# Optimization experiments

Measured on AMD Instinct MI355X. Metric: run time of the kernel, lower is better.

The kernel has to match this reference:

```python
import jax, jax.numpy as jnp
import numpy as np

B, T, D, H = 32, 8192, 128, 128

def setup_inputs() -> dict:
    key = jax.random.key(0)
    k1, k2, k3, k4, k5 = jax.random.split(key, 5)
    return {
        "encoder_outputs": jax.random.normal(k1, (B, T, D), dtype=jnp.float32),
        "decoder_hidden": jax.random.normal(k2, (B, H), dtype=jnp.float32),
        "W1": jax.random.normal(k3, (D, D), dtype=jnp.float32) * 0.08,
        "W2": jax.random.normal(k4, (H, D), dtype=jnp.float32) * 0.08,
        "V": jax.random.normal(k5, (D, 1), dtype=jnp.float32) * 0.08,
    }

def reference(encoder_outputs, decoder_hidden, W1, W2, V):
    # score: [B, T, D] = tanh(enc @ W1 + (dec @ W2)[:, None, :])
    score = jnp.tanh(jnp.einsum('btd,de->bte', encoder_outputs, W1)
                     + jnp.einsum('bh,hd->bd', decoder_hidden, W2)[:, None, :])
    # logits: [B, T, 1]; softmax over time axis (axis=1)
    logits = jnp.einsum('btd,do->bto', score, V)
    attention_weights = jax.nn.softmax(logits, axis=1)
    # context: [B, D] weighted sum over T
    context_vector = jnp.sum(attention_weights * encoder_outputs, axis=1)
    return context_vector, attention_weights
```

## Files before the change

### kernel.cpp

```cpp
#include <hip/hip_runtime.h>

#define B_ 32
#define T_ 8192
#define D_ 128
#define MBLK 128
#define NCHUNK 64

typedef __attribute__((ext_vector_type(8))) _Float16 half8;
typedef __attribute__((ext_vector_type(4))) _Float16 half4;
typedef __attribute__((ext_vector_type(4))) float floatx4;

__device__ __forceinline__ float tanh_fast(float x) {
    float e = __expf(2.0f * x);
    return 1.0f - __fdividef(2.0f, e + 1.0f);
}

__global__ void prep_kernel(const float* __restrict__ W1, half8* __restrict__ W1frag,
                            const float* __restrict__ dec, const float* __restrict__ W2,
                            float* __restrict__ bias) {
    int bid = blockIdx.x, tid = threadIdx.x;
    if (bid < 8) {
        int tg = bid * 256 + tid;
        int kk = tg >> 9, ni = (tg >> 6) & 7, lane = tg & 63;
        half8 h;
        #pragma unroll
        for (int j = 0; j < 8; ++j) {
            int k = kk * 32 + ((lane >> 4) * 8) + j;
            int n = ni * 16 + (lane & 15);
            h[j] = (_Float16)W1[k * 128 + n];
        }
        W1frag[tg] = h;
    } else {
        int b = (bid - 8) * 2 + (tid >> 7);
        int d = tid & 127;
        float acc = 0.f;
        for (int h = 0; h < 128; ++h)
            acc += dec[b * 128 + h] * W2[h * 128 + d];
        bias[b * 128 + d] = acc;
    }
}

__global__ __launch_bounds__(512, 4)
void main_kernel(const float* __restrict__ enc, const half8* __restrict__ W1frag,
                 const float* __restrict__ bias, const float* __restrict__ V,
                 float* __restrict__ out_w, float* __restrict__ m_part,
                 float* __restrict__ s_part, float* __restrict__ c_part)
{
    __shared__ __align__(16) _Float16 encl[MBLK * 128];
    __shared__ __align__(16) half8 bfr[2048];
    __shared__ float red[MBLK];
    __shared__ float c_red[16][128];

    const int tid = threadIdx.x;
    const int l = tid & 63;
    const int w = tid >> 6;
    const int bid = blockIdx.x;
    const int b = bid >> 6;
    const int chunk = bid & 63;
    const float* encp = enc + ((long)(b * T_) + chunk * MBLK) * D_;

    #pragma unroll
    for (int q = 0; q < 4; ++q)
        bfr[q * 512 + tid] = W1frag[q * 512 + tid];

    const int arow = w * 16 + (l & 15);
    const float* rowp = encp + arow * 128 + ((l >> 4) * 8);
    half8 afr[4];
    #pragma unroll
    for (int kk = 0; kk < 4; ++kk) {
        float4 f0 = *(const float4*)(rowp + kk * 32);
        float4 f1 = *(const float4*)(rowp + kk * 32 + 4);
        half8 a;
        a[0] = (_Float16)f0.x; a[1] = (_Float16)f0.y;
        a[2] = (_Float16)f0.z; a[3] = (_Float16)f0.w;
        a[4] = (_Float16)f1.x; a[5] = (_Float16)f1.y;
        a[6] = (_Float16)f1.z; a[7] = (_Float16)f1.w;
        afr[kk] = a;
    }
    __syncthreads();

    floatx4 acc[8];
    #pragma unroll
    for (int ni = 0; ni < 8; ++ni) acc[ni] = (floatx4)0.0f;

    #pragma unroll
    for (int kk = 0; kk < 4; ++kk)
        #pragma unroll
        for (int ni = 0; ni < 8; ++ni)
            acc[ni] = __builtin_amdgcn_mfma_f32_16x16x32_f16(
                          afr[kk], bfr[(kk * 8 + ni) * 64 + l], acc[ni], 0, 0, 0);

    {
        const int asw = (arow & 7) << 4;
        #pragma unroll
        for (int kk = 0; kk < 4; ++kk) {
            int byte = arow * 256 + (((kk * 64) + ((l >> 4) * 16)) ^ asw);
            *(half8*)((char*)encl + byte) = afr[kk];
        }
    }

    float bs[8], vv[8];
    #pragma unroll
    for (int ni = 0; ni < 8; ++ni) {
        int n = ni * 16 + (l & 15);
        bs[ni] = bias[b * 128 + n];
        vv[ni] = V[n];
    }
    #pragma unroll
    for (int j2 = 0; j2 < 4; ++j2) {
        float p = 0.f;
        #pragma unroll
        for (int ni = 0; ni < 8; ++ni)
            p += tanh_fast(acc[ni][j2] + bs[ni]) * vv[ni];
        #pragma unroll
        for (int mk = 1; mk < 16; mk <<= 1)
            p += __shfl_xor(p, mk);
        if ((l & 15) == 0) {
            int r = w * 16 + (l >> 4) * 4 + j2;
            red[r] = p;
            out_w[(long)b * T_ + chunk * MBLK + r] = p;
        }
    }
    __syncthreads();

    float l0 = red[l], l1 = red[l + 64];
    float m = fmaxf(l0, l1);
    #pragma unroll
    for (int mk = 1; mk < 64; mk <<= 1) m = fmaxf(m, __shfl_xor(m, mk));
    {
        float e0 = __expf(l0 - m), e1 = __expf(l1 - m);
        float s = e0 + e1;
        #pragma unroll
        for (int mk = 1; mk < 64; mk <<= 1) s += __shfl_xor(s, mk);
        if (tid == 0) { m_part[bid] = m; s_part[bid] = s; }
    }

    {
        int dg = tid & 31, rg = tid >> 5;
        floatx4 cc = (floatx4)0.0f;
        #pragma unroll
        for (int rr = 0; rr < 8; ++rr) {
            int r = rg * 8 + rr;
            float wgt = __expf(red[r] - m);
            half4 h = *(const half4*)((char*)encl +
                       (r * 256 + ((dg * 8) ^ ((r & 7) << 4))));
            #pragma unroll
            for (int i = 0; i < 4; ++i) cc[i] += wgt * (float)h[i];
        }
        *(floatx4*)(&c_red[rg][dg * 4]) = cc;
    }
    __syncthreads();
    if (tid < 128) {
        float s = 0.f;
        #pragma unroll
        for (int g = 0; g < 16; ++g) s += c_red[g][tid];
        c_part[(long)bid * 128 + tid] = s;
    }
}

__global__ void reduce_kernel(const float* __restrict__ m_part, const float* __restrict__ s_part,
                              const float* __restrict__ c_part, float* __restrict__ ctx,
                              float* __restrict__ mg, float* __restrict__ sg)
{
    __shared__ float sm[64];
    __shared__ float sc[64];
    int b = blockIdx.x, i = threadIdx.x;
    float m = m_part[b * 64 + i];
    sm[i] = m;
    __syncthreads();
    for (int s = 32; s > 0; s >>= 1) {
        if (i < s) sm[i] = fmaxf(sm[i], sm[i + s]);
        __syncthreads();
    }
    float m_g = sm[0];
    __syncthreads();
    float e = __expf(m - m_g);
    sm[i] = s_part[b * 64 + i] * e;
    __syncthreads();
    for (int s = 32; s > 0; s >>= 1) {
        if (i < s) sm[i] += sm[i + s];
        __syncthreads();
    }
    float s_g = sm[0];
    __syncthreads();
    sc[i] = e / s_g;
    if (i == 0) { mg[b] = m_g; sg[b] = s_g; }
    __syncthreads();
    float acc0 = 0.f, acc1 = 0.f;
    for (int ch = 0; ch < 64; ++ch) {
        float w = sc[ch];
        acc0 += c_part[((long)b * 64 + ch) * 128 + i] * w;
        acc1 += c_part[((long)b * 64 + ch) * 128 + 64 + i] * w;
    }
    ctx[b * 128 + i] = acc0;
    ctx[b * 128 + 64 + i] = acc1;
}

__global__ void finalize_kernel(float* __restrict__ out_w, const float* __restrict__ mg,
                                const float* __restrict__ sg)
{
    int idx = blockIdx.x * 256 + threadIdx.x;
    int b = idx >> 13;
    float lg = out_w[idx];
    out_w[idx] = __expf(lg - mg[b]) / sg[b];
}

extern "C" void kernel_launch(void* const* d_in, const int* in_sizes, int n_in,
                              void* d_out, int out_size, void* d_ws, size_t ws_size,
                              hipStream_t stream)
{
    const float* enc = (const float*)d_in[0];
    const float* dec = (const float*)d_in[1];
    const float* W1  = (const float*)d_in[2];
    const float* W2  = (const float*)d_in[3];
    const float* V   = (const float*)d_in[4];

    float* ctx  = (float*)d_out;
    float* outw = ctx + B_ * D_;

    float* ws     = (float*)d_ws;
    float* bias   = ws;
    float* m_part = bias + 4096;
    float* s_part = m_part + 2048;
    float* mg     = s_part + 2048;
    float* sg     = mg + 32;
    float* c_part = sg + 32;
    half8* W1frag = (half8*)(c_part + (long)B_ * NCHUNK * 128);

    prep_kernel<<<24, 256, 0, stream>>>(W1, W1frag, dec, W2, bias);
    main_kernel<<<B_ * NCHUNK, 512, 0, stream>>>(enc, W1frag, bias, V, outw, m_part, s_part, c_part);
    reduce_kernel<<<B_, 64, 0, stream>>>(m_part, s_part, c_part, ctx, mg, sg);
    finalize_kernel<<<(B_ * T_) / 256, 256, 0, stream>>>(outw, mg, sg);
}
```

Baseline: 54.62 us.

## Drop LDS staging of encoder tile, fuse finalize into reduce kernel

The context accumulation now uses the fp16 A fragments already held in registers, reduced with cross-lane shuffles, so the 32KB LDS copy of the encoder tile and its swizzled write/read are removed. Global loads of enc, W1 fragments and bias are issued before a single barrier. The finalize kernel is folded into the reduce kernel, which uses wave shuffles instead of LDS tree reductions and saves one launch. This cuts LDS use and may raise occupancy, at the cost of more shuffle instructions and only 32 blocks doing the attention-weight normalization pass.

```diff
diff --git a/kernel.cpp b/kernel.cpp
--- a/kernel.cpp
+++ b/kernel.cpp
@@ -7,7 +7,6 @@
 #define NCHUNK 64
 
 typedef __attribute__((ext_vector_type(8))) _Float16 half8;
-typedef __attribute__((ext_vector_type(4))) _Float16 half4;
 typedef __attribute__((ext_vector_type(4))) float floatx4;
 
 __device__ __forceinline__ float tanh_fast(float x) {
@@ -40,31 +39,27 @@
     }
 }
 
-__global__ __launch_bounds__(512, 4)
+__global__ __launch_bounds__(512)
 void main_kernel(const float* __restrict__ enc, const half8* __restrict__ W1frag,
                  const float* __restrict__ bias, const float* __restrict__ V,
                  float* __restrict__ out_w, float* __restrict__ m_part,
                  float* __restrict__ s_part, float* __restrict__ c_part)
 {
-    __shared__ __align__(16) _Float16 encl[MBLK * 128];
     __shared__ __align__(16) half8 bfr[2048];
-    __shared__ float red[MBLK];
-    __shared__ float c_red[16][128];
+    __shared__ __align__(16) float red[MBLK];
+    __shared__ __align__(16) float c_red[8][128];
 
     const int tid = threadIdx.x;
     const int l = tid & 63;
     const int w = tid >> 6;
+    const int g = l >> 4;
     const int bid = blockIdx.x;
     const int b = bid >> 6;
     const int chunk = bid & 63;
     const float* encp = enc + ((long)(b * T_) + chunk * MBLK) * D_;
 
-    #pragma unroll
-    for (int q = 0; q < 4; ++q)
-        bfr[q * 512 + tid] = W1frag[q * 512 + tid];
-
     const int arow = w * 16 + (l & 15);
-    const float* rowp = encp + arow * 128 + ((l >> 4) * 8);
+    const float* rowp = encp + arow * 128 + g * 8;
     half8 afr[4];
     #pragma unroll
     for (int kk = 0; kk < 4; ++kk) {
@@ -77,27 +72,10 @@
         a[6] = (_Float16)f1.z; a[7] = (_Float16)f1.w;
         afr[kk] = a;
     }
-    __syncthreads();
-
-    floatx4 acc[8];
-    #pragma unroll
-    for (int ni = 0; ni < 8; ++ni) acc[ni] = (floatx4)0.0f;
-
-    #pragma unroll
-    for (int kk = 0; kk < 4; ++kk)
-        #pragma unroll
-        for (int ni = 0; ni < 8; ++ni)
-            acc[ni] = __builtin_amdgcn_mfma_f32_16x16x32_f16(
-                          afr[kk], bfr[(kk * 8 + ni) * 64 + l], acc[ni], 0, 0, 0);
-
-    {
-        const int asw = (arow & 7) << 4;
-        #pragma unroll
-        for (int kk = 0; kk < 4; ++kk) {
-            int byte = arow * 256 + (((kk * 64) + ((l >> 4) * 16)) ^ asw);
-            *(half8*)((char*)encl + byte) = afr[kk];
-        }
-    }
+
+    #pragma unroll
+    for (int q = 0; q < 4; ++q)
+        bfr[q * 512 + tid] = W1frag[q * 512 + tid];
 
     float bs[8], vv[8];
     #pragma unroll
@@ -106,20 +84,35 @@
         bs[ni] = bias[b * 128 + n];
         vv[ni] = V[n];
     }
+    __syncthreads();
+
+    floatx4 acc[8];
+    #pragma unroll
+    for (int ni = 0; ni < 8; ++ni) acc[ni] = (floatx4)0.0f;
+
+    #pragma unroll
+    for (int kk = 0; kk < 4; ++kk)
+        #pragma unroll
+        for (int ni = 0; ni < 8; ++ni)
+            acc[ni] = __builtin_amdgcn_mfma_f32_16x16x32_f16(
+                          afr[kk], bfr[(kk * 8 + ni) * 64 + l], acc[ni], 0, 0, 0);
+
+    float p[4];
     #pragma unroll
     for (int j2 = 0; j2 < 4; ++j2) {
-        float p = 0.f;
+        float q = 0.f;
         #pragma unroll
         for (int ni = 0; ni < 8; ++ni)
-            p += tanh_fast(acc[ni][j2] + bs[ni]) * vv[ni];
+            q += tanh_fast(acc[ni][j2] + bs[ni]) * vv[ni];
         #pragma unroll
         for (int mk = 1; mk < 16; mk <<= 1)
-            p += __shfl_xor(p, mk);
-        if ((l & 15) == 0) {
-            int r = w * 16 + (l >> 4) * 4 + j2;
-            red[r] = p;
-            out_w[(long)b * T_ + chunk * MBLK + r] = p;
-        }
+            q += __shfl_xor(q, mk);
+        p[j2] = q;
+    }
+    if ((l & 15) == 0) {
+        floatx4 v4 = {p[0], p[1], p[2], p[3]};
+        *(floatx4*)(&red[w * 16 + g * 4]) = v4;
+        *(floatx4*)(out_w + (long)b * T_ + chunk * MBLK + w * 16 + g * 4) = v4;
     }
     __syncthreads();
 
@@ -128,81 +121,76 @@
     #pragma unroll
     for (int mk = 1; mk < 64; mk <<= 1) m = fmaxf(m, __shfl_xor(m, mk));
     {
-        float e0 = __expf(l0 - m), e1 = __expf(l1 - m);
-        float s = e0 + e1;
+        float s = __expf(l0 - m) + __expf(l1 - m);
         #pragma unroll
         for (int mk = 1; mk < 64; mk <<= 1) s += __shfl_xor(s, mk);
         if (tid == 0) { m_part[bid] = m; s_part[bid] = s; }
     }
 
     {
-        int dg = tid & 31, rg = tid >> 5;
-        floatx4 cc = (floatx4)0.0f;
-        #pragma unroll
-        for (int rr = 0; rr < 8; ++rr) {
-            int r = rg * 8 + rr;
-            float wgt = __expf(red[r] - m);
-            half4 h = *(const half4*)((char*)encl +
-                       (r * 256 + ((dg * 8) ^ ((r & 7) << 4))));
+        float wgt = __expf(red[arow] - m);
+        #pragma unroll
+        for (int kk = 0; kk < 4; ++kk) {
+            float cc[8];
             #pragma unroll
-            for (int i = 0; i < 4; ++i) cc[i] += wgt * (float)h[i];
+            for (int j = 0; j < 8; ++j) {
+                cc[j] = wgt * (float)afr[kk][j];
+                #pragma unroll
+                for (int mk = 1; mk < 16; mk <<= 1)
+                    cc[j] += __shfl_xor(cc[j], mk);
+            }
+            if ((l & 15) == 0) {
+                floatx4 v0 = {cc[0], cc[1], cc[2], cc[3]};
+                floatx4 v1 = {cc[4], cc[5], cc[6], cc[7]};
+                *(floatx4*)(&c_red[w][kk * 32 + g * 8]) = v0;
+                *(floatx4*)(&c_red[w][kk * 32 + g * 8 + 4]) = v1;
+            }
         }
-        *(floatx4*)(&c_red[rg][dg * 4]) = cc;
     }
     __syncthreads();
     if (tid < 128) {
         float s = 0.f;
         #pragma unroll
-        for (int g = 0; g < 16; ++g) s += c_red[g][tid];
+        for (int ww = 0; ww < 8; ++ww) s += c_red[ww][tid];
         c_part[(long)bid * 128 + tid] = s;
     }
 }
 
-__global__ void reduce_kernel(const float* __restrict__ m_part, const float* __restrict__ s_part,
-                              const float* __restrict__ c_part, float* __restrict__ ctx,
-                              float* __restrict__ mg, float* __restrict__ sg)
+__global__ __launch_bounds__(256)
+void reduce_kernel(const float* __restrict__ m_part, const float* __restrict__ s_part,
+                   const float* __restrict__ c_part, float* __restrict__ ctx,
+                   float* __restrict__ out_w)
 {
-    __shared__ float sm[64];
     __shared__ float sc[64];
-    int b = blockIdx.x, i = threadIdx.x;
-    float m = m_part[b * 64 + i];
-    sm[i] = m;
-    __syncthreads();
-    for (int s = 32; s > 0; s >>= 1) {
-        if (i < s) sm[i] = fmaxf(sm[i], sm[i + s]);
-        __syncthreads();
-    }
-    float m_g = sm[0];
-    __syncthreads();
-    float e = __expf(m - m_g);
-    sm[i] = s_part[b * 64 + i] * e;
-    __syncthreads();
-    for (int s = 32; s > 0; s >>= 1) {
-        if (i < s) sm[i] += sm[i + s];
-        __syncthreads();
-    }
-    float s_g = sm[0];
-    __syncthreads();
-    sc[i] = e / s_g;
-    if (i == 0) { mg[b] = m_g; sg[b] = s_g; }
-    __syncthreads();
-    float acc0 = 0.f, acc1 = 0.f;
-    for (int ch = 0; ch < 64; ++ch) {
-        float w = sc[ch];
-        acc0 += c_part[((long)b * 64 + ch) * 128 + i] * w;
-        acc1 += c_part[((long)b * 64 + ch) * 128 + 64 + i] * w;
-    }
-    ctx[b * 128 + i] = acc0;
-    ctx[b * 128 + 64 + i] = acc1;
-}
-
-__global__ void finalize_kernel(float* __restrict__ out_w, const float* __restrict__ mg,
-                                const float* __restrict__ sg)
-{
-    int idx = blockIdx.x * 256 + threadIdx.x;
-    int b = idx >> 13;
-    float lg = out_w[idx];
-    out_w[idx] = __expf(lg - mg[b]) / sg[b];
+    __shared__ float stats[2];
+    int b = blockIdx.x, tid = threadIdx.x;
+
+    if (tid < 64) {
+        float m = m_part[b * 64 + tid];
+        float mg = m;
+        #pragma unroll
+        for (int mk = 1; mk < 64; mk <<= 1) mg = fmaxf(mg, __shfl_xor(mg, mk));
+        float e = __expf(m - mg);
+        float s = s_part[b * 64 + tid] * e;
+        #pragma unroll
+        for (int mk = 1; mk < 64; mk <<= 1) s += __shfl_xor(s, mk);
+        sc[tid] = e;
+        if (tid == 0) { stats[0] = mg; stats[1] = s; }
+    }
+    __syncthreads();
+    float m_g = stats[0], s_g = stats[1];
+    float inv = __fdividef(1.0f, s_g);
+
+    if (tid < 128) {
+        float acc = 0.f;
+        for (int ch = 0; ch < 64; ++ch)
+            acc += c_part[((long)b * 64 + ch) * 128 + tid] * sc[ch];
+        ctx[b * 128 + tid] = acc * inv;
+    }
+
+    float* ow = out_w + (long)b * T_;
+    for (int i = tid; i < T_; i += 256)
+        ow[i] = __expf(ow[i] - m_g) * inv;
 }
 
 extern "C" void kernel_launch(void* const* d_in, const int* in_sizes, int n_in,
@@ -222,13 +210,10 @@
     float* bias   = ws;
     float* m_part = bias + 4096;
     float* s_part = m_part + 2048;
-    float* mg     = s_part + 2048;
-    float* sg     = mg + 32;
-    float* c_part = sg + 32;
+    float* c_part = s_part + 2048;
     half8* W1frag = (half8*)(c_part + (long)B_ * NCHUNK * 128);
 
     prep_kernel<<<24, 256, 0, stream>>>(W1, W1frag, dec, W2, bias);
     main_kernel<<<B_ * NCHUNK, 512, 0, stream>>>(enc, W1frag, bias, V, outw, m_part, s_part, c_part);
-    reduce_kernel<<<B_, 64, 0, stream>>>(m_part, s_part, c_part, ctx, mg, sg);
-    finalize_kernel<<<(B_ * T_) / 256, 256, 0, stream>>>(outw, mg, sg);
-}
+    reduce_kernel<<<B_, 256, 0, stream>>>(m_part, s_part, c_part, ctx, outw);
+}
```

New measurement: 73.05 us. +33.8%, slower.
